# Optimization experiments

Measured on AMD Instinct MI355X. Metric: run time of the kernel, lower is better.

Reference implementation:

```python
import jax, jax.numpy as jnp
import numpy as np

# DenseCRFHead hyperparameters (init_kwargs)
WEIGHT = 1e-8
SIGMA_RGB = 15.0
SIGMA_XY = 100.0
SCALE = 0.5


def setup_inputs() -> dict:
    key = jax.random.key(0)
    k1, k2 = jax.random.split(key)
    N, C, H, W = 8, 3, 64, 64          # images already at scaled resolution
    K, Hs, Ws = 21, 128, 128           # segmentations at full resolution
    images = jax.random.uniform(k1, (N, C, H, W), dtype=jnp.float32) * 255.0
    segmentations = jax.random.uniform(k2, (N, K, Hs, Ws), dtype=jnp.float32)
    return {"images": images, "segmentations": segmentations}


def reference(images, segmentations):
    N, K, H2, W2 = segmentations.shape
    H, W = int(H2 * SCALE), int(W2 * SCALE)
    P = H * W

    # F.interpolate(..., scale_factor, mode='bilinear', align_corners=False)
    seg = jax.image.resize(segmentations, (N, K, H, W), method="bilinear")
    segf = seg.reshape(N, K, P)

    # images are not differentiated in the original custom Function (grad None)
    img = jax.lax.stop_gradient(images)

    # bilateral features: spatial scaled by sigma_xy*scale_factor, color by sigma_rgb
    sxy = SIGMA_XY * SCALE
    ys, xs = jnp.meshgrid(jnp.arange(H, dtype=jnp.float32),
                          jnp.arange(W, dtype=jnp.float32), indexing="ij")
    pos = jnp.stack([xs, ys], axis=-1).reshape(P, 2) / sxy          # [P,2]
    col = img.reshape(N, 3, P).transpose(0, 2, 1) / SIGMA_RGB       # [N,P,3]

    d_xy = jnp.sum((pos[:, None, :] - pos[None, :, :]) ** 2, axis=-1)  # [P,P]

    def per_image(args):
        cn, sn = args                                   # [P,3], [K,P]
        d_rgb = jnp.sum((cn[:, None, :] - cn[None, :, :]) ** 2, axis=-1)
        Wk = jnp.exp(-0.5 * (d_xy + d_rgb))             # [P,P] bilateral kernel
        return jnp.einsum("ij,kj->ki", Wk, sn)          # AS = W @ seg

    # sequential over batch keeps peak memory to one [P,P] kernel
    AS = jax.lax.map(per_image, (col, segf))            # [N,K,P]

    loss = -jnp.sum(segf * AS) / N
    return (WEIGHT * loss).reshape(1)
```

## Files before the change

### kernel.cpp

```cpp
#include <hip/hip_runtime.h>

#define NP   4096
#define NIMG 8
#define NK   21
#define ROWH 32
#define NT   16
#define ITEMS_PER_IMG 136
#define N_HALF (NIMG * ITEMS_PER_IMG * 2)
#define GRID2 1024
#define GSTRIDE 2064
#define ASTRIDE 8256
#define BUFSTRIDE 16512

#define FEAT_SCALE 0.84932180028801907f

typedef _Float16 half8 __attribute__((ext_vector_type(8)));
typedef float f32x4 __attribute__((ext_vector_type(4)));

__device__ __forceinline__ unsigned short h2u(_Float16 h) {
  union { _Float16 f; unsigned short u; } c; c.f = h; return c.u;
}

__device__ __forceinline__ void resize_w(int o, float* w, int* t) {
  const float ww[4] = {0.25f, 0.75f, 0.75f, 0.25f};
  float s = 0.f;
  #pragma unroll
  for (int a = 0; a < 4; ++a) {
    int tap = 2 * o - 1 + a;
    bool v = (tap >= 0) && (tap < 128);
    w[a] = v ? ww[a] : 0.f;
    t[a] = v ? tap : 0;
    s += w[a];
  }
  float inv = 1.f / s;
  #pragma unroll
  for (int a = 0; a < 4; ++a) w[a] *= inv;
}

__global__ void __launch_bounds__(256) prep_kernel(const float* __restrict__ images,
                                                   const float* __restrict__ segs,
                                                   _Float16* __restrict__ distA,
                                                   _Float16* __restrict__ distB,
                                                   _Float16* __restrict__ segh) {
  int bid = blockIdx.x;
  int tid = threadIdx.x;
  int n = bid / 112;
  int r112 = bid % 112;
  int oyg = r112 / 7, kq = r112 % 7;
  int ox = tid & 63, oyl = tid >> 6;
  int oy = oyg * 4 + oyl;
  int p = oy * 64 + ox;
  int idx = n * NP + p;

  if (kq == 0) {
    const float cxy  = FEAT_SCALE / 50.0f;
    const float crgb = FEAT_SCALE / 15.0f;
    const float* img = images + (size_t)n * 3 * NP;
    float f[5];
    f[0] = (float)ox * cxy;
    f[1] = (float)oy * cxy;
    f[2] = img[0 * NP + p] * crgb;
    f[3] = img[1 * NP + p] * crgb;
    f[4] = img[2 * NP + p] * crgb;

    _Float16 ah[5], al[5];
    float n2 = 0.f;
    #pragma unroll
    for (int d = 0; d < 5; ++d) {
      ah[d] = (_Float16)f[d];
      float rem = f[d] - (float)ah[d];
      al[d] = (_Float16)rem;
      float at = (float)ah[d] + (float)al[d];
      n2 = fmaf(at, at, n2);
    }
    _Float16 nh = (_Float16)n2;
    _Float16 nl = (_Float16)(n2 - (float)nh);

    _Float16 rowA[ROWH], rowB[ROWH];
    #pragma unroll
    for (int q = 0; q < ROWH; ++q) { rowA[q] = (_Float16)0.f; rowB[q] = (_Float16)0.f; }
    #pragma unroll
    for (int d = 0; d < 5; ++d) {
      rowA[d]      = ah[d];
      rowA[5 + d]  = al[d];
      rowA[10 + d] = ah[d];
      rowB[d]      = (_Float16)2.f * ah[d];
      rowB[5 + d]  = (_Float16)2.f * ah[d];
      rowB[10 + d] = (_Float16)2.f * al[d];
    }
    rowA[15] = nh;  rowA[16] = nl;  rowA[17] = (_Float16)1.f; rowA[18] = (_Float16)1.f;
    rowB[15] = (_Float16)-1.f; rowB[16] = (_Float16)-1.f; rowB[17] = -nh; rowB[18] = -nl;

    half8* oA = (half8*)(distA + (size_t)idx * ROWH);
    half8* oB = (half8*)(distB + (size_t)idx * ROWH);
    #pragma unroll
    for (int q = 0; q < 4; ++q) {
      oA[q] = ((half8*)rowA)[q];
      oB[q] = ((half8*)rowB)[q];
    }
  }

  __shared__ float slab[2][10][128];
  int r0 = 8 * oyg - 1;
  float wy[4], wx[4]; int ty[4], tx[4];
  resize_w(oy, wy, ty);
  resize_w(ox, wx, tx);

  int lofs[5], lrr[5], lcc[5];
  #pragma unroll
  for (int q = 0; q < 5; ++q) {
    int e = tid + q * 256;
    int rr = e >> 7, cc = e & 127;
    int row = r0 + rr;
    row = row < 0 ? 0 : (row > 127 ? 127 : row);
    lofs[q] = row * 128 + cc;
    lrr[q] = rr; lcc[q] = cc;
  }

  const float* sb = segs + (size_t)n * NK * 128 * 128;
  float rg[5];
  {
    const float* sk = sb + (size_t)(kq * 3) * 128 * 128;
    #pragma unroll
    for (int q = 0; q < 5; ++q) rg[q] = sk[lofs[q]];
    #pragma unroll
    for (int q = 0; q < 5; ++q) slab[0][lrr[q]][lcc[q]] = rg[q];
  }

  float outk[3];
  #pragma unroll
  for (int kk = 0; kk < 3; ++kk) {
    if (kk < 2) {
      const float* sk = sb + (size_t)(kq * 3 + kk + 1) * 128 * 128;
      #pragma unroll
      for (int q = 0; q < 5; ++q) rg[q] = sk[lofs[q]];
    }
    __syncthreads();
    float a = 0.f;
    #pragma unroll
    for (int ay = 0; ay < 4; ++ay) {
      int rel = 2 * oyl + ay;
      float rsum = 0.f;
      #pragma unroll
      for (int ax = 0; ax < 4; ++ax) rsum = fmaf(wx[ax], slab[kk & 1][rel][tx[ax]], rsum);
      a = fmaf(wy[ay], rsum, a);
    }
    outk[kk] = a;
    if (kk < 2) {
      #pragma unroll
      for (int q = 0; q < 5; ++q) slab[(kk & 1) ^ 1][lrr[q]][lcc[q]] = rg[q];
    }
  }

  char* rowp = (char*)(segh + (size_t)idx * ROWH);
  #pragma unroll
  for (int kk = 0; kk < 3; ++kk)
    *(unsigned short*)(rowp + 6 * kq + 2 * kk) = h2u((_Float16)outk[kk]);
  if (kq == 6) {
    *(unsigned short*)    (rowp + 42) = 0;
    *(unsigned int*)      (rowp + 44) = 0u;
    *(unsigned long long*)(rowp + 48) = 0ull;
    *(unsigned long long*)(rowp + 56) = 0ull;
  }
}

__device__ __forceinline__ void decode_item(int item, int& n, int& I, int& J, int& h) {
  h = item & 1;
  int pr = item >> 1;
  n = pr / ITEMS_PER_IMG;
  int rem = pr - n * ITEMS_PER_IMG;
  int I_ = 0;
  while (rem >= NT - I_) { rem -= NT - I_; ++I_; }
  I = I_;
  J = I_ + rem;
}

__global__ void __launch_bounds__(256, 4) crf_mfma(const _Float16* __restrict__ distA,
                                                   const _Float16* __restrict__ distB,
                                                   const _Float16* __restrict__ segh,
                                                   float* __restrict__ slots) {
  __shared__ char lds[2 * BUFSTRIDE];
  __shared__ float red[4];
  int bid = blockIdx.x;
  int tid = threadIdx.x;
  int lane = tid & 63, wid = tid >> 6;
  int r = lane & 15, g4 = lane >> 4;

  int item = bid;
  int n, I, J, h;
  decode_item(item, n, I, J, h);

  float4 rd0, rd1, rs0, rs1;
  {
    const char* srcBd = (const char*)(distB + (size_t)n * NP * ROWH) + (size_t)(J * 256 + h * 128) * 64;
    const char* srcBs = (const char*)(segh  + (size_t)n * NP * ROWH) + (size_t)(J * 256 + h * 128) * 64;
    rd0 = *(const float4*)(srcBd + tid * 16);
    rd1 = *(const float4*)(srcBd + tid * 16 + 4096);
    rs0 = *(const float4*)(srcBs + tid * 16);
    rs1 = *(const float4*)(srcBs + tid * 16 + 4096);
  }
  {
    int e0 = tid, e1 = tid + 256;
    int d0 = (e0 & 3) * GSTRIDE + (e0 >> 2) * 16;
    int d1 = (e1 & 3) * GSTRIDE + (e1 >> 2) * 16;
    *(float4*)(lds + d0) = rd0;
    *(float4*)(lds + d1) = rd1;
    *(float4*)(lds + ASTRIDE + d0) = rs0;
    *(float4*)(lds + ASTRIDE + d1) = rs1;
  }

  float blocksum = 0.f;
  int cur = 0;
  f32x4 zero = {0.f, 0.f, 0.f, 0.f};

  #pragma unroll 1
  for (;;) {
    int nxt = item + GRID2;
    bool more = (nxt < N_HALF);
    int nn = 0, nI = 0, nJ = 0, nh = 0;

    const char* dAn = (const char*)(distA + (size_t)n * NP * ROWH);
    const char* sgn = (const char*)(segh  + (size_t)n * NP * ROWH);
    half8 Ad[4], As[4];
    #pragma unroll
    for (int m = 0; m < 4; ++m) {
      size_t aoff = (size_t)(I * 256 + (wid * 4 + m) * 16 + r) * 64 + g4 * 16;
      Ad[m] = *(const half8*)(dAn + aoff);
      As[m] = *(const half8*)(sgn + aoff);
    }

    if (more) {
      decode_item(nxt, nn, nI, nJ, nh);
      const char* srcBd = (const char*)(distB + (size_t)nn * NP * ROWH) + (size_t)(nJ * 256 + nh * 128) * 64;
      const char* srcBs = (const char*)(segh  + (size_t)nn * NP * ROWH) + (size_t)(nJ * 256 + nh * 128) * 64;
      rd0 = *(const float4*)(srcBd + tid * 16);
      rd1 = *(const float4*)(srcBd + tid * 16 + 4096);
      rs0 = *(const float4*)(srcBs + tid * 16);
      rs1 = *(const float4*)(srcBs + tid * 16 + 4096);
    }

    __syncthreads();

    const char* buf = lds + cur * BUFSTRIDE;
    float sm0 = 0.f, sm1 = 0.f, sm2 = 0.f, sm3 = 0.f;

    if (J > I) {
      #pragma unroll 4
      for (int jt = 0; jt < 8; ++jt) {
        const char* bp = buf + g4 * GSTRIDE + (jt * 16 + r) * 16;
        half8 Bd = *(const half8*)bp;
        half8 Bs = *(const half8*)(bp + ASTRIDE);
        #pragma unroll
        for (int m = 0; m < 4; ++m) {
          f32x4 ad  = __builtin_amdgcn_mfma_f32_16x16x32_f16(Ad[m], Bd, zero, 0, 0, 0);
          f32x4 as_ = __builtin_amdgcn_mfma_f32_16x16x32_f16(As[m], Bs, zero, 0, 0, 0);
          float t0 = fmaf(__builtin_amdgcn_exp2f(ad[0]), as_[0],
                     fmaf(__builtin_amdgcn_exp2f(ad[1]), as_[1], 0.f));
          float t1 = fmaf(__builtin_amdgcn_exp2f(ad[2]), as_[2],
                     fmaf(__builtin_amdgcn_exp2f(ad[3]), as_[3], 0.f));
          float t = 2.f * (t0 + t1);
          if (m == 0) sm0 += t; else if (m == 1) sm1 += t;
          else if (m == 2) sm2 += t; else sm3 += t;
        }
      }
    } else {
      #pragma unroll 2
      for (int jt = 0; jt < 8; ++jt) {
        int jta = I * 16 + h * 8 + jt;
        const char* bp = buf + g4 * GSTRIDE + (jt * 16 + r) * 16;
        half8 Bd = *(const half8*)bp;
        half8 Bs = *(const half8*)(bp + ASTRIDE);
        #pragma unroll
        for (int m = 0; m < 4; ++m) {
          int it = I * 16 + wid * 4 + m;
          if (jta >= it) {
            float s = (jta > it) ? 2.f : 1.f;
            f32x4 ad  = __builtin_amdgcn_mfma_f32_16x16x32_f16(Ad[m], Bd, zero, 0, 0, 0);
            f32x4 as_ = __builtin_amdgcn_mfma_f32_16x16x32_f16(As[m], Bs, zero, 0, 0, 0);
            float t0 = fmaf(__builtin_amdgcn_exp2f(ad[0]), as_[0],
                       fmaf(__builtin_amdgcn_exp2f(ad[1]), as_[1], 0.f));
            float t1 = fmaf(__builtin_amdgcn_exp2f(ad[2]), as_[2],
                       fmaf(__builtin_amdgcn_exp2f(ad[3]), as_[3], 0.f));
            float t = s * (t0 + t1);
            if (m == 0) sm0 += t; else if (m == 1) sm1 += t;
            else if (m == 2) sm2 += t; else sm3 += t;
          }
        }
      }
    }
    blocksum += sm0 + sm1 + sm2 + sm3;

    if (!more) break;

    {
      char* nbuf = lds + (cur ^ 1) * BUFSTRIDE;
      int e0 = tid, e1 = tid + 256;
      int d0 = (e0 & 3) * GSTRIDE + (e0 >> 2) * 16;
      int d1 = (e1 & 3) * GSTRIDE + (e1 >> 2) * 16;
      *(float4*)(nbuf + d0) = rd0;
      *(float4*)(nbuf + d1) = rd1;
      *(float4*)(nbuf + ASTRIDE + d0) = rs0;
      *(float4*)(nbuf + ASTRIDE + d1) = rs1;
    }
    item = nxt; n = nn; I = nI; J = nJ; h = nh; cur ^= 1;
  }

  #pragma unroll
  for (int off = 32; off > 0; off >>= 1) blocksum += __shfl_down(blocksum, off);
  if (lane == 0) red[wid] = blocksum;
  __syncthreads();
  if (tid == 0) slots[bid] = red[0] + red[1] + red[2] + red[3];
}

__global__ void __launch_bounds__(256) reduce_kernel(const float* __restrict__ slots,
                                                     float* __restrict__ out) {
  __shared__ double dred[4];
  int tid = threadIdx.x;
  int lane = tid & 63, wid = tid >> 6;
  double s = 0.0;
  #pragma unroll
  for (int q = 0; q < 4; ++q) s += (double)slots[tid + q * 256];
  #pragma unroll
  for (int off = 32; off > 0; off >>= 1) s += __shfl_down(s, off);
  if (lane == 0) dred[wid] = s;
  __syncthreads();
  if (tid == 0) {
    double tot = dred[0] + dred[1] + dred[2] + dred[3];
    out[0] = (float)(tot * (-1e-8 / 8.0));
  }
}

extern "C" void kernel_launch(void* const* d_in, const int* in_sizes, int n_in,
                              void* d_out, int out_size, void* d_ws, size_t ws_size,
                              hipStream_t stream) {
  const float* images = (const float*)d_in[0];
  const float* segs   = (const float*)d_in[1];
  float* out  = (float*)d_out;
  float* slots = (float*)d_ws;
  _Float16* distA = (_Float16*)((char*)d_ws + 16384);
  _Float16* distB = distA + (size_t)NIMG * NP * ROWH;
  _Float16* segh  = distB + (size_t)NIMG * NP * ROWH;

  hipLaunchKernelGGL(prep_kernel, dim3(NIMG * 16 * 7), dim3(256), 0, stream,
                     images, segs, distA, distB, segh);
  hipLaunchKernelGGL(crf_mfma, dim3(GRID2), dim3(256), 0, stream,
                     distA, distB, segh, slots);
  hipLaunchKernelGGL(reduce_kernel, dim3(1), dim3(256), 0, stream, slots, out);
}
```

Measured before the change: 33.14 us.

## Prefetch next A fragments in registers and split prep across all channels

```diff
diff --git a/kernel.cpp b/kernel.cpp
--- a/kernel.cpp
+++ b/kernel.cpp
@@ -44,13 +44,30 @@
                                                    _Float16* __restrict__ segh) {
   int bid = blockIdx.x;
   int tid = threadIdx.x;
-  int n = bid / 112;
-  int r112 = bid % 112;
-  int oyg = r112 / 7, kq = r112 % 7;
+  int n = bid / 336;
+  int r336 = bid % 336;
+  int oyg = r336 / 21, kq = r336 % 21;
   int ox = tid & 63, oyl = tid >> 6;
   int oy = oyg * 4 + oyl;
   int p = oy * 64 + ox;
   int idx = n * NP + p;
+
+  __shared__ float slab[10][128];
+  int r0 = 8 * oyg - 1;
+  int lofs[5], lrr[5], lcc[5];
+  #pragma unroll
+  for (int q = 0; q < 5; ++q) {
+    int e = tid + q * 256;
+    int rr = e >> 7, cc = e & 127;
+    int row = r0 + rr;
+    row = row < 0 ? 0 : (row > 127 ? 127 : row);
+    lofs[q] = row * 128 + cc;
+    lrr[q] = rr; lcc[q] = cc;
+  }
+  const float* sk = segs + ((size_t)n * NK + kq) * 128 * 128;
+  float rg[5];
+  #pragma unroll
+  for (int q = 0; q < 5; ++q) rg[q] = sk[lofs[q]];
 
   if (kq == 0) {
     const float cxy  = FEAT_SCALE / 50.0f;
@@ -100,63 +117,26 @@
     }
   }
 
-  __shared__ float slab[2][10][128];
-  int r0 = 8 * oyg - 1;
+  #pragma unroll
+  for (int q = 0; q < 5; ++q) slab[lrr[q]][lcc[q]] = rg[q];
   float wy[4], wx[4]; int ty[4], tx[4];
   resize_w(oy, wy, ty);
   resize_w(ox, wx, tx);
-
-  int lofs[5], lrr[5], lcc[5];
-  #pragma unroll
-  for (int q = 0; q < 5; ++q) {
-    int e = tid + q * 256;
-    int rr = e >> 7, cc = e & 127;
-    int row = r0 + rr;
-    row = row < 0 ? 0 : (row > 127 ? 127 : row);
-    lofs[q] = row * 128 + cc;
-    lrr[q] = rr; lcc[q] = cc;
-  }
-
-  const float* sb = segs + (size_t)n * NK * 128 * 128;
-  float rg[5];
-  {
-    const float* sk = sb + (size_t)(kq * 3) * 128 * 128;
-    #pragma unroll
-    for (int q = 0; q < 5; ++q) rg[q] = sk[lofs[q]];
-    #pragma unroll
-    for (int q = 0; q < 5; ++q) slab[0][lrr[q]][lcc[q]] = rg[q];
-  }
-
-  float outk[3];
-  #pragma unroll
-  for (int kk = 0; kk < 3; ++kk) {
-    if (kk < 2) {
-      const float* sk = sb + (size_t)(kq * 3 + kk + 1) * 128 * 128;
-      #pragma unroll
-      for (int q = 0; q < 5; ++q) rg[q] = sk[lofs[q]];
-    }
-    __syncthreads();
-    float a = 0.f;
-    #pragma unroll
-    for (int ay = 0; ay < 4; ++ay) {
-      int rel = 2 * oyl + ay;
-      float rsum = 0.f;
-      #pragma unroll
-      for (int ax = 0; ax < 4; ++ax) rsum = fmaf(wx[ax], slab[kk & 1][rel][tx[ax]], rsum);
-      a = fmaf(wy[ay], rsum, a);
-    }
-    outk[kk] = a;
-    if (kk < 2) {
-      #pragma unroll
-      for (int q = 0; q < 5; ++q) slab[(kk & 1) ^ 1][lrr[q]][lcc[q]] = rg[q];
-    }
+  __syncthreads();
+
+  float a = 0.f;
+  #pragma unroll
+  for (int ay = 0; ay < 4; ++ay) {
+    int rel = 2 * oyl + ay;
+    float rsum = 0.f;
+    #pragma unroll
+    for (int ax = 0; ax < 4; ++ax) rsum = fmaf(wx[ax], slab[rel][tx[ax]], rsum);
+    a = fmaf(wy[ay], rsum, a);
   }
 
   char* rowp = (char*)(segh + (size_t)idx * ROWH);
-  #pragma unroll
-  for (int kk = 0; kk < 3; ++kk)
-    *(unsigned short*)(rowp + 6 * kq + 2 * kk) = h2u((_Float16)outk[kk]);
-  if (kq == 6) {
+  *(unsigned short*)(rowp + 2 * kq) = h2u((_Float16)a);
+  if (kq == 20) {
     *(unsigned short*)    (rowp + 42) = 0;
     *(unsigned int*)      (rowp + 44) = 0u;
     *(unsigned long long*)(rowp + 48) = 0ull;
@@ -199,15 +179,27 @@
     rs0 = *(const float4*)(srcBs + tid * 16);
     rs1 = *(const float4*)(srcBs + tid * 16 + 4096);
   }
+  half8 Ad[4], As[4];
   {
-    int e0 = tid, e1 = tid + 256;
-    int d0 = (e0 & 3) * GSTRIDE + (e0 >> 2) * 16;
+    const char* dAn = (const char*)(distA + (size_t)n * NP * ROWH);
+    const char* sgn = (const char*)(segh  + (size_t)n * NP * ROWH);
+    #pragma unroll
+    for (int m = 0; m < 4; ++m) {
+      size_t aoff = (size_t)(I * 256 + (wid * 4 + m) * 16 + r) * 64 + g4 * 16;
+      Ad[m] = *(const half8*)(dAn + aoff);
+      As[m] = *(const half8*)(sgn + aoff);
+    }
+  }
+  {
+    int d0 = (tid & 3) * GSTRIDE + (tid >> 2) * 16;
+    int e1 = tid + 256;
     int d1 = (e1 & 3) * GSTRIDE + (e1 >> 2) * 16;
     *(float4*)(lds + d0) = rd0;
     *(float4*)(lds + d1) = rd1;
     *(float4*)(lds + ASTRIDE + d0) = rs0;
     *(float4*)(lds + ASTRIDE + d1) = rs1;
   }
+  __syncthreads();
 
   float blocksum = 0.f;
   int cur = 0;
@@ -218,16 +210,7 @@
     int nxt = item + GRID2;
     bool more = (nxt < N_HALF);
     int nn = 0, nI = 0, nJ = 0, nh = 0;
-
-    const char* dAn = (const char*)(distA + (size_t)n * NP * ROWH);
-    const char* sgn = (const char*)(segh  + (size_t)n * NP * ROWH);
-    half8 Ad[4], As[4];
-    #pragma unroll
-    for (int m = 0; m < 4; ++m) {
-      size_t aoff = (size_t)(I * 256 + (wid * 4 + m) * 16 + r) * 64 + g4 * 16;
-      Ad[m] = *(const half8*)(dAn + aoff);
-      As[m] = *(const half8*)(sgn + aoff);
-    }
+    half8 nAd[4], nAs[4];
 
     if (more) {
       decode_item(nxt, nn, nI, nJ, nh);
@@ -237,9 +220,15 @@
       rd1 = *(const float4*)(srcBd + tid * 16 + 4096);
       rs0 = *(const float4*)(srcBs + tid * 16);
       rs1 = *(const float4*)(srcBs + tid * 16 + 4096);
-    }
-
-    __syncthreads();
+      const char* dAn = (const char*)(distA + (size_t)nn * NP * ROWH);
+      const char* sgn = (const char*)(segh  + (size_t)nn * NP * ROWH);
+      #pragma unroll
+      for (int m = 0; m < 4; ++m) {
+        size_t aoff = (size_t)(nI * 256 + (wid * 4 + m) * 16 + r) * 64 + g4 * 16;
+        nAd[m] = *(const half8*)(dAn + aoff);
+        nAs[m] = *(const half8*)(sgn + aoff);
+      }
+    }
 
     const char* buf = lds + cur * BUFSTRIDE;
     float sm0 = 0.f, sm1 = 0.f, sm2 = 0.f, sm3 = 0.f;
@@ -294,14 +283,18 @@
 
     {
       char* nbuf = lds + (cur ^ 1) * BUFSTRIDE;
-      int e0 = tid, e1 = tid + 256;
-      int d0 = (e0 & 3) * GSTRIDE + (e0 >> 2) * 16;
+      int d0 = (tid & 3) * GSTRIDE + (tid >> 2) * 16;
+      int e1 = tid + 256;
       int d1 = (e1 & 3) * GSTRIDE + (e1 >> 2) * 16;
       *(float4*)(nbuf + d0) = rd0;
       *(float4*)(nbuf + d1) = rd1;
       *(float4*)(nbuf + ASTRIDE + d0) = rs0;
       *(float4*)(nbuf + ASTRIDE + d1) = rs1;
     }
+    __syncthreads();
+
+    #pragma unroll
+    for (int m = 0; m < 4; ++m) { Ad[m] = nAd[m]; As[m] = nAs[m]; }
     item = nxt; n = nn; I = nI; J = nJ; h = nh; cur ^= 1;
   }
 
@@ -341,7 +334,7 @@
   _Float16* distB = distA + (size_t)NIMG * NP * ROWH;
   _Float16* segh  = distB + (size_t)NIMG * NP * ROWH;
 
-  hipLaunchKernelGGL(prep_kernel, dim3(NIMG * 16 * 7), dim3(256), 0, stream,
+  hipLaunchKernelGGL(prep_kernel, dim3(NIMG * 16 * 21), dim3(256), 0, stream,
                      images, segs, distA, distB, segh);
   hipLaunchKernelGGL(crf_mfma, dim3(GRID2), dim3(256), 0, stream,
                      distA, distB, segh, slots);
```

Result: slower. 37.47 us (+13.0%).
